# Kernel optimization log

Measured on AMD Instinct MI355X. Metric: run time of the kernel, lower is better.

Reference implementation:

```python
import jax, jax.numpy as jnp
import numpy as np

TAU = 0.07
EPS = 1e-6
N_SRC, N_TGT, D = 65536, 1024, 256
N_CLASSES = 345


def setup_inputs() -> dict:
    key = jax.random.key(0)
    k1, k2, k3 = jax.random.split(key, 3)
    source_features = jax.random.normal(k1, (N_SRC, D), dtype=jnp.float32)
    target_features = jax.random.normal(k2, (N_TGT, D), dtype=jnp.float32)
    source_labels = jax.random.randint(k3, (N_SRC,), 0, N_CLASSES)
    return {
        "source_features": source_features,
        "source_labels": source_labels,
        "target_features": target_features,
        "ranking_k": 5,
        "top_ranked_n": 512,
        "top_n_sim": 5,
    }


def _mode_along0(x):
    # torch.mode(dim=0): most frequent value; ties broken by smallest value.
    # x: [K, T] int. counts[i, t] = #{j : x[j,t] == x[i,t]}
    counts = (x[:, None, :] == x[None, :, :]).sum(axis=1)  # [K, T]
    # lexicographic key: maximize count, then minimize value
    score = counts.astype(jnp.int32) * 1000000 - x
    best = jnp.argmax(score, axis=0)  # [T]
    return jnp.take_along_axis(x, best[None, :], axis=0)[0]


def reference(source_features, source_labels, target_features, ranking_k, top_ranked_n, top_n_sim):
    # cosine similarity matrix [N_src, N_tgt]
    s = source_features / jnp.linalg.norm(source_features, axis=1, keepdims=True)
    t = target_features / jnp.linalg.norm(target_features, axis=1, keepdims=True)
    sim = s @ t.T

    # sort each column descending (over source axis)
    order = jnp.argsort(-sim, axis=0)                      # [Ns, Nt]
    sim_sorted = jnp.take_along_axis(sim, order, axis=0)   # [Ns, Nt]

    # kNN pseudo-label per target: mode of top_n_sim nearest source labels
    neigh = source_labels[order[:top_n_sim]]               # [K, Nt]
    assigned = _mode_along0(neigh)                         # [Nt]

    # per-target confidence score: sum of top-ranking_k same-label sims /
    #                              sum of top-ranking_k diff-label sims (in sorted order)
    lbl_sorted = source_labels[order]                      # [Ns, Nt]
    m = lbl_sorted == assigned[None, :]                    # [Ns, Nt] bool
    nln = jnp.where(m & (jnp.cumsum(m, axis=0) <= ranking_k), sim_sorted, 0.0).sum(axis=0)
    nm = ~m
    nun = jnp.where(nm & (jnp.cumsum(nm, axis=0) <= ranking_k), sim_sorted, 0.0).sum(axis=0)
    scores = jax.lax.stop_gradient(nln / nun)              # [Nt] (detached in original)

    # keep top_ranked_n most confident targets
    _, idx = jax.lax.top_k(scores, top_ranked_n)           # [Ntop]
    csim = sim[:, idx]                                     # [Ns, Ntop]
    clab = assigned[idx]                                   # [Ntop]

    # masked contrastive loss over source axis
    mask = (source_labels[:, None] == clab[None, :]).astype(csim.dtype)
    p = jax.nn.softmax(csim / TAU, axis=0)
    contrast = (p * mask).sum(axis=0) / p.sum(axis=0)
    return -jnp.mean(jnp.log(contrast + EPS))
```

## Files before the change

kernel.cpp:

```cpp
#include <hip/hip_runtime.h>
#include <cmath>
#include <cstdint>
#include <cstddef>
#include <climits>

#define N_SRC 65536
#define N_TGT 1024
#define DIM   256
#define TAU_INV (1.0f/0.07f)
#define LOSS_EPS 1e-6f
#define TOPSEL 512
#define N_CLASSES 345
#define SLICE_R 256
#define NS (N_SRC/SLICE_R)

typedef __bf16 bf16x8 __attribute__((ext_vector_type(8)));
typedef float  f32x4  __attribute__((ext_vector_type(4)));

__device__ __forceinline__ unsigned short f2bf(float x) {
  unsigned u = __float_as_uint(x);
  unsigned r = (u + 0x7fffu + ((u >> 16) & 1u)) >> 16;
  return (unsigned short)r;
}
__device__ __forceinline__ float bf2f(unsigned short h) {
  return __uint_as_float(((unsigned)h) << 16);
}

__device__ __forceinline__ void insert5_vi(float v[5], int id[5], float nv, int ni) {
  bool beats_last = (nv > v[4]) || (nv == v[4] && ni < id[4]);
  if (!beats_last) return;
  #pragma unroll
  for (int p = 4; p > 0; --p) {
    bool up = (nv > v[p-1]) || (nv == v[p-1] && ni < id[p-1]);
    if (up) { v[p] = v[p-1]; id[p] = id[p-1]; }
    else    { v[p] = nv; id[p] = ni; return; }
  }
  v[0] = nv; id[0] = ni;
}
__device__ __forceinline__ void insert5_v(float v[5], float nv) {
  if (!(nv > v[4])) return;
  #pragma unroll
  for (int p = 4; p > 0; --p) {
    if (nv > v[p-1]) v[p] = v[p-1];
    else { v[p] = nv; return; }
  }
  v[0] = nv;
}
__device__ __forceinline__ void wave_merge5_vi(float v[5], int id[5]) {
  #pragma unroll
  for (int off = 1; off < 64; off <<= 1) {
    float pv[5]; int pi[5];
    #pragma unroll
    for (int u = 0; u < 5; ++u) {
      pv[u] = __shfl_xor(v[u], off, 64);
      pi[u] = __shfl_xor(id[u], off, 64);
    }
    #pragma unroll
    for (int u = 0; u < 5; ++u) insert5_vi(v, id, pv[u], pi[u]);
  }
}
__device__ __forceinline__ void wave_merge5_v(float v[5]) {
  #pragma unroll
  for (int off = 1; off < 64; off <<= 1) {
    float pv[5];
    #pragma unroll
    for (int u = 0; u < 5; ++u) pv[u] = __shfl_xor(v[u], off, 64);
    #pragma unroll
    for (int u = 0; u < 5; ++u) insert5_v(v, pv[u]);
  }
}

__global__ __launch_bounds__(512) void k_zero(int* __restrict__ hist) {
  if (threadIdx.x < N_CLASSES) hist[threadIdx.x] = 0;
}
__global__ __launch_bounds__(256) void k_hist(const int* __restrict__ labels,
                                              int* __restrict__ hist) {
  int i = blockIdx.x * 256 + threadIdx.x;
  atomicAdd(&hist[labels[i]], 1);
}
__global__ __launch_bounds__(64) void k_scan(const int* __restrict__ hist,
                                             int* __restrict__ start,
                                             int* __restrict__ cursor) {
  if (threadIdx.x == 0) {
    int acc = 0;
    for (int c = 0; c < N_CLASSES; ++c) {
      start[c] = acc; cursor[c] = acc; acc += hist[c];
    }
    start[N_CLASSES] = acc;
  }
}
__global__ __launch_bounds__(256) void k_perm(const int* __restrict__ labels,
                                              int* __restrict__ cursor,
                                              int* __restrict__ g,
                                              int* __restrict__ sortedLab) {
  int i = blockIdx.x * 256 + threadIdx.x;
  int l = labels[i];
  int slot = atomicAdd(&cursor[l], 1);
  g[slot] = i;
  sortedLab[slot] = l;
}

__global__ __launch_bounds__(256) void k_norm_split(const float* __restrict__ X,
                                                    const int* __restrict__ g,
                                                    unsigned short* __restrict__ hi,
                                                    unsigned short* __restrict__ lo) {
  int wave = threadIdx.x >> 6, lane = threadIdx.x & 63;
  int row  = blockIdx.x * 4 + wave;
  int src  = g ? g[row] : row;
  float4 v = reinterpret_cast<const float4*>(X + (size_t)src * DIM)[lane];
  float ss = v.x*v.x + v.y*v.y + v.z*v.z + v.w*v.w;
  #pragma unroll
  for (int o = 32; o > 0; o >>= 1) ss += __shfl_xor(ss, o, 64);
  float r = 1.0f / sqrtf(ss);
  v.x *= r; v.y *= r; v.z *= r; v.w *= r;
  ushort4 h, l;
  h.x = f2bf(v.x); l.x = f2bf(v.x - bf2f(h.x));
  h.y = f2bf(v.y); l.y = f2bf(v.y - bf2f(h.y));
  h.z = f2bf(v.z); l.z = f2bf(v.z - bf2f(h.z));
  h.w = f2bf(v.w); l.w = f2bf(v.w - bf2f(h.w));
  reinterpret_cast<ushort4*>(hi + (size_t)row * DIM)[lane] = h;
  reinterpret_cast<ushort4*>(lo + (size_t)row * DIM)[lane] = l;
}

__device__ __forceinline__ void gl_lds(const unsigned short* g, unsigned short* d) {
  __builtin_amdgcn_global_load_lds(
      (const __attribute__((address_space(1))) unsigned int*)g,
      (__attribute__((address_space(3))) unsigned int*)d, 16, 0, 0);
}

__global__ __launch_bounds__(256) void k_gemm(
    const unsigned short* __restrict__ Ahi, const unsigned short* __restrict__ Alo,
    const unsigned short* __restrict__ Bhi, const unsigned short* __restrict__ Blo,
    float* __restrict__ simIJ, int cols, int j_off)
{
  __shared__ unsigned short As_hi[128*32];
  __shared__ unsigned short As_lo[128*32];
  __shared__ unsigned short Bs_hi[128*32];
  __shared__ unsigned short Bs_lo[128*32];

  const int tid  = threadIdx.x;
  const int lane = tid & 63;
  const int w    = tid >> 6;
  const int wm   = w & 1;
  const int wn   = w >> 1;
  const int i0   = blockIdx.x * 128;
  const int j0g  = j_off + blockIdx.y * 128;
  const int j0l  = blockIdx.y * 128;

  f32x4 acc[4][4];
  #pragma unroll
  for (int a = 0; a < 4; ++a)
    #pragma unroll
    for (int b = 0; b < 4; ++b) acc[a][b] = f32x4{0.f, 0.f, 0.f, 0.f};

  const int srow = (w << 5) + (lane >> 2);
  const int scol = (lane & 3) << 3;
  const unsigned short* gAh = Ahi + (size_t)(j0g + srow) * DIM + scol;
  const unsigned short* gAl = Alo + (size_t)(j0g + srow) * DIM + scol;
  const unsigned short* gBh = Bhi + (size_t)(i0  + srow) * DIM + scol;
  const unsigned short* gBl = Blo + (size_t)(i0  + srow) * DIM + scol;
  unsigned short* dA0  = &As_hi[(w << 5) * 32];
  unsigned short* dA1  = &As_hi[((w << 5) + 16) * 32];
  unsigned short* dB0  = &Bs_hi[(w << 5) * 32];
  unsigned short* dB1  = &Bs_hi[((w << 5) + 16) * 32];
  unsigned short* dA0l = &As_lo[(w << 5) * 32];
  unsigned short* dA1l = &As_lo[((w << 5) + 16) * 32];
  unsigned short* dB0l = &Bs_lo[(w << 5) * 32];
  unsigned short* dB1l = &Bs_lo[((w << 5) + 16) * 32];

  const int fr = lane & 15;
  const int fk = (lane >> 4) << 3;

  for (int k0 = 0; k0 < DIM; k0 += 32) {
    __syncthreads();
    gl_lds(gAh + k0,           dA0);
    gl_lds(gAh + k0 + 16*DIM,  dA1);
    gl_lds(gAl + k0,           dA0l);
    gl_lds(gAl + k0 + 16*DIM,  dA1l);
    gl_lds(gBh + k0,           dB0);
    gl_lds(gBh + k0 + 16*DIM,  dB1);
    gl_lds(gBl + k0,           dB0l);
    gl_lds(gBl + k0 + 16*DIM,  dB1l);
    __syncthreads();

    bf16x8 ah[4], al[4], bh[4], bl[4];
    #pragma unroll
    for (int rf = 0; rf < 4; ++rf) {
      int r = ((wm << 6) + (rf << 4) + fr) * 32 + fk;
      ah[rf] = *(const bf16x8*)&As_hi[r];
      al[rf] = *(const bf16x8*)&As_lo[r];
    }
    #pragma unroll
    for (int cf = 0; cf < 4; ++cf) {
      int r = ((wn << 6) + (cf << 4) + fr) * 32 + fk;
      bh[cf] = *(const bf16x8*)&Bs_hi[r];
      bl[cf] = *(const bf16x8*)&Bs_lo[r];
    }
    #pragma unroll
    for (int rf = 0; rf < 4; ++rf)
      #pragma unroll
      for (int cf = 0; cf < 4; ++cf) {
        acc[rf][cf] = __builtin_amdgcn_mfma_f32_16x16x32_bf16(ah[rf], bh[cf], acc[rf][cf], 0, 0, 0);
        acc[rf][cf] = __builtin_amdgcn_mfma_f32_16x16x32_bf16(ah[rf], bl[cf], acc[rf][cf], 0, 0, 0);
        acc[rf][cf] = __builtin_amdgcn_mfma_f32_16x16x32_bf16(al[rf], bh[cf], acc[rf][cf], 0, 0, 0);
      }
  }

  #pragma unroll
  for (int rf = 0; rf < 4; ++rf) {
    const int m_base = (wm << 6) + (rf << 4) + ((lane >> 4) << 2);
    #pragma unroll
    for (int cf = 0; cf < 4; ++cf) {
      const int n = (wn << 6) + (cf << 4) + (lane & 15);
      *reinterpret_cast<float4*>(&simIJ[(size_t)(i0 + n) * cols + j0l + m_base]) =
          make_float4(acc[rf][cf][0], acc[rf][cf][1], acc[rf][cf][2], acc[rf][cf][3]);
    }
  }
}

template<int CPT>
__global__ __launch_bounds__(512) void k_part1t(const float* __restrict__ sim,
                                                int cols,
                                                float* __restrict__ p1v,
                                                int* __restrict__ p1i,
                                                float* __restrict__ pse) {
  const int s  = blockIdx.x;
  const int t  = threadIdx.x;
  const int jc = t * CPT;
  if (jc >= cols) return;
  float tv0[5]; int ti0[5]; float se0 = 0.f;
  float tv1[5]; int ti1[5]; float se1 = 0.f;
  #pragma unroll
  for (int u = 0; u < 5; ++u) { tv0[u] = -INFINITY; ti0[u] = INT_MAX;
                                tv1[u] = -INFINITY; ti1[u] = INT_MAX; }
  const int i0 = s * SLICE_R;
  #pragma unroll 4
  for (int it = 0; it < SLICE_R; ++it) {
    const int i = i0 + it;
    if constexpr (CPT == 2) {
      float2 v = *reinterpret_cast<const float2*>(&sim[(size_t)i * cols + jc]);
      se0 += __expf(v.x * TAU_INV);
      se1 += __expf(v.y * TAU_INV);
      if (v.x > tv0[4]) insert5_vi(tv0, ti0, v.x, i);
      if (v.y > tv1[4]) insert5_vi(tv1, ti1, v.y, i);
    } else {
      float v = sim[(size_t)i * cols + jc];
      se0 += __expf(v * TAU_INV);
      if (v > tv0[4]) insert5_vi(tv0, ti0, v, i);
    }
  }
  {
    const size_t o = ((size_t)s * cols + jc) * 5;
    #pragma unroll
    for (int u = 0; u < 5; ++u) { p1v[o+u] = tv0[u]; p1i[o+u] = ti0[u]; }
    pse[(size_t)s * cols + jc] = se0;
  }
  if constexpr (CPT == 2) {
    const size_t o = ((size_t)s * cols + jc + 1) * 5;
    #pragma unroll
    for (int u = 0; u < 5; ++u) { p1v[o+u] = tv1[u]; p1i[o+u] = ti1[u]; }
    pse[(size_t)s * cols + jc + 1] = se1;
  }
}

__global__ __launch_bounds__(256) void k_assign(const float* __restrict__ p1v,
                                                const int* __restrict__ p1i,
                                                const int* __restrict__ sortedLab,
                                                int* __restrict__ assigned,
                                                int cols, int j_off) {
  const int w = threadIdx.x >> 6, lane = threadIdx.x & 63;
  const int jloc = blockIdx.x * 4 + w;
  float v[5]; int id[5];
  #pragma unroll
  for (int u = 0; u < 5; ++u) { v[u] = -INFINITY; id[u] = INT_MAX; }
  #pragma unroll
  for (int r = 0; r < NS/64; ++r) {
    const int s = r * 64 + lane;
    const size_t o = ((size_t)s * cols + jloc) * 5;
    #pragma unroll
    for (int u = 0; u < 5; ++u) insert5_vi(v, id, p1v[o+u], p1i[o+u]);
  }
  wave_merge5_vi(v, id);
  if (lane == 0) {
    int lab[5];
    #pragma unroll
    for (int a = 0; a < 5; ++a) lab[a] = sortedLab[id[a]];
    int bestSc = INT_MIN, bestA = 0;
    #pragma unroll
    for (int a = 0; a < 5; ++a) {
      int c = 0;
      #pragma unroll
      for (int b = 0; b < 5; ++b) c += (lab[b] == lab[a]) ? 1 : 0;
      int sc = c * 1000000 - lab[a];
      if (sc > bestSc) { bestSc = sc; bestA = a; }
    }
    assigned[j_off + jloc] = lab[bestA];
  }
}

__global__ __launch_bounds__(256) void k_part2n(const float* __restrict__ sim,
                                                const int* __restrict__ assigned,
                                                const int* __restrict__ start,
                                                const float* __restrict__ p1v,
                                                const float* __restrict__ pse,
                                                float* __restrict__ scores,
                                                float* __restrict__ contrast,
                                                int cols, int j_off) {
  const int w = threadIdx.x >> 6, lane = threadIdx.x & 63;
  const int jloc = blockIdx.x * 4 + w;
  const int j    = j_off + jloc;
  const int asg  = assigned[j];
  const int a    = start[asg];
  const int b    = start[asg + 1];
  const int s0   = a >> 8;
  const int s1   = (b - 1) >> 8;

  float mt[5], ut[5]; float sem = 0.f, se = 0.f;
  #pragma unroll
  for (int u = 0; u < 5; ++u) { mt[u] = -INFINITY; ut[u] = -INFINITY; }

  for (int i = s0 * SLICE_R + lane; i < (s1 + 1) * SLICE_R; i += 64) {
    float v = sim[(size_t)i * cols + jloc];
    if (i >= a && i < b) { sem += __expf(v * TAU_INV); insert5_v(mt, v); }
    else insert5_v(ut, v);
  }
  #pragma unroll
  for (int r = 0; r < NS/64; ++r) {
    const int s = r * 64 + lane;
    se += pse[(size_t)s * cols + jloc];
    if (s < s0 || s > s1) {
      const size_t o = ((size_t)s * cols + jloc) * 5;
      #pragma unroll
      for (int u = 0; u < 5; ++u) insert5_v(ut, p1v[o+u]);
    }
  }
  #pragma unroll
  for (int o = 32; o > 0; o >>= 1) { sem += __shfl_xor(sem, o, 64); se += __shfl_xor(se, o, 64); }
  wave_merge5_v(mt);
  wave_merge5_v(ut);
  if (lane == 0) {
    float nln = 0.f, nun = 0.f;
    #pragma unroll
    for (int u = 0; u < 5; ++u) {
      if (mt[u] > -1e30f) nln += mt[u];
      if (ut[u] > -1e30f) nun += ut[u];
    }
    scores[j]   = nln / nun;
    contrast[j] = sem / se;
  }
}

__global__ __launch_bounds__(1024) void k_finalize(const float* __restrict__ scores,
                                                   const float* __restrict__ contrast,
                                                   float* __restrict__ out) {
  __shared__ float sc[N_TGT];
  __shared__ float red[N_TGT];
  const int j = threadIdx.x;
  sc[j] = scores[j];
  __syncthreads();
  float my = sc[j];
  int rank = 0;
  for (int m = 0; m < N_TGT; ++m) {
    float s = sc[m];
    rank += ((s > my) || (s == my && m < j)) ? 1 : 0;
  }
  red[j] = (rank < TOPSEL) ? logf(contrast[j] + LOSS_EPS) : 0.0f;
  __syncthreads();
  for (int s = 512; s > 0; s >>= 1) { if (j < s) red[j] += red[j+s]; __syncthreads(); }
  if (j == 0) out[0] = -red[0] / (float)TOPSEL;
}

extern "C" void kernel_launch(void* const* d_in, const int* in_sizes, int n_in,
                              void* d_out, int out_size, void* d_ws, size_t ws_size,
                              hipStream_t stream) {
  const float* S      = (const float*)d_in[0];
  const int*   labels = (const int*)d_in[1];
  const float* T      = (const float*)d_in[2];
  float* out = (float*)d_out;

  float* ws = (float*)d_ws;
  float* scores    = ws;
  float* contrastA = scores + N_TGT;
  int*   assigned  = (int*)(contrastA + N_TGT);
  float* p1v       = (float*)(assigned + N_TGT);
  int*   p1i       = (int*)(p1v + (size_t)NS*N_TGT*5);
  float* pse       = (float*)(p1i + (size_t)NS*N_TGT*5);
  int*   hist      = (int*)(pse + (size_t)NS*N_TGT);
  int*   startArr  = hist + N_CLASSES;
  int*   cursor    = startArr + (N_CLASSES + 1);
  int*   gidx      = cursor + N_CLASSES;
  int*   sortedLab = gidx + N_SRC;
  unsigned short* Shi = (unsigned short*)(sortedLab + N_SRC);
  unsigned short* Slo = Shi + (size_t)N_SRC*DIM;
  unsigned short* Thi = Slo + (size_t)N_SRC*DIM;
  unsigned short* Tlo = Thi + (size_t)N_TGT*DIM;
  float* simbuf       = (float*)(Tlo + (size_t)N_TGT*DIM);

  size_t head  = (size_t)(simbuf - ws);
  size_t avail = (ws_size / 4 > head) ? (ws_size / 4 - head) : 0;
  int cols = 128;
  if      (avail >= (size_t)1024 * N_SRC) cols = 1024;
  else if (avail >= (size_t)512  * N_SRC) cols = 512;
  else if (avail >= (size_t)256  * N_SRC) cols = 256;

  k_zero<<<1, 512, 0, stream>>>(hist);
  k_hist<<<N_SRC/256, 256, 0, stream>>>(labels, hist);
  k_scan<<<1, 64, 0, stream>>>(hist, startArr, cursor);
  k_perm<<<N_SRC/256, 256, 0, stream>>>(labels, cursor, gidx, sortedLab);

  k_norm_split<<<N_TGT/4, 256, 0, stream>>>(T, nullptr, Thi, Tlo);
  k_norm_split<<<N_SRC/4, 256, 0, stream>>>(S, gidx, Shi, Slo);

  for (int j_off = 0; j_off < N_TGT; j_off += cols) {
    dim3 gg(N_SRC / 128, cols / 128);
    k_gemm<<<gg, 256, 0, stream>>>(Thi, Tlo, Shi, Slo, simbuf, cols, j_off);
    if (cols >= 1024)
      k_part1t<2><<<NS, 512, 0, stream>>>(simbuf, cols, p1v, p1i, pse);
    else
      k_part1t<1><<<NS, 512, 0, stream>>>(simbuf, cols, p1v, p1i, pse);
    k_assign<<<cols/4, 256, 0, stream>>>(p1v, p1i, sortedLab, assigned, cols, j_off);
    k_part2n<<<cols/4, 256, 0, stream>>>(simbuf, assigned, startArr, p1v, pse,
                                         scores, contrastA, cols, j_off);
  }
  k_finalize<<<1, 1024, 0, stream>>>(scores, contrastA, out);
}
```

Measured before the change: 1.098 ms.

## Shrink partial-reduction slices, swizzle GEMM block order, use one column per thread

```diff
diff --git a/kernel.cpp b/kernel.cpp
--- a/kernel.cpp
+++ b/kernel.cpp
@@ -11,7 +11,7 @@
 #define LOSS_EPS 1e-6f
 #define TOPSEL 512
 #define N_CLASSES 345
-#define SLICE_R 256
+#define SLICE_R 64
 #define NS (N_SRC/SLICE_R)
 
 typedef __bf16 bf16x8 __attribute__((ext_vector_type(8)));
@@ -143,9 +143,16 @@
   const int w    = tid >> 6;
   const int wm   = w & 1;
   const int wn   = w >> 1;
-  const int i0   = blockIdx.x * 128;
-  const int j0g  = j_off + blockIdx.y * 128;
-  const int j0l  = blockIdx.y * 128;
+
+  const int nby = cols >> 7;
+  const int d   = blockIdx.x;
+  const int c   = d & 7;
+  const int kk  = d >> 3;
+  const int by  = kk % nby;
+  const int bx  = (kk / nby) * 8 + c;
+  const int i0   = bx * 128;
+  const int j0g  = j_off + by * 128;
+  const int j0l  = by * 128;
 
   f32x4 acc[4][4];
   #pragma unroll
@@ -218,49 +225,28 @@
   }
 }
 
-template<int CPT>
-__global__ __launch_bounds__(512) void k_part1t(const float* __restrict__ sim,
-                                                int cols,
-                                                float* __restrict__ p1v,
-                                                int* __restrict__ p1i,
-                                                float* __restrict__ pse) {
+__global__ __launch_bounds__(1024) void k_part1t(const float* __restrict__ sim,
+                                                 int cols,
+                                                 float* __restrict__ p1v,
+                                                 int* __restrict__ p1i,
+                                                 float* __restrict__ pse) {
   const int s  = blockIdx.x;
-  const int t  = threadIdx.x;
-  const int jc = t * CPT;
-  if (jc >= cols) return;
+  const int jc = threadIdx.x;
   float tv0[5]; int ti0[5]; float se0 = 0.f;
-  float tv1[5]; int ti1[5]; float se1 = 0.f;
-  #pragma unroll
-  for (int u = 0; u < 5; ++u) { tv0[u] = -INFINITY; ti0[u] = INT_MAX;
-                                tv1[u] = -INFINITY; ti1[u] = INT_MAX; }
+  #pragma unroll
+  for (int u = 0; u < 5; ++u) { tv0[u] = -INFINITY; ti0[u] = INT_MAX; }
   const int i0 = s * SLICE_R;
-  #pragma unroll 4
+  const float* p = sim + (size_t)i0 * cols + jc;
+  #pragma unroll 8
   for (int it = 0; it < SLICE_R; ++it) {
-    const int i = i0 + it;
-    if constexpr (CPT == 2) {
-      float2 v = *reinterpret_cast<const float2*>(&sim[(size_t)i * cols + jc]);
-      se0 += __expf(v.x * TAU_INV);
-      se1 += __expf(v.y * TAU_INV);
-      if (v.x > tv0[4]) insert5_vi(tv0, ti0, v.x, i);
-      if (v.y > tv1[4]) insert5_vi(tv1, ti1, v.y, i);
-    } else {
-      float v = sim[(size_t)i * cols + jc];
-      se0 += __expf(v * TAU_INV);
-      if (v > tv0[4]) insert5_vi(tv0, ti0, v, i);
-    }
-  }
-  {
-    const size_t o = ((size_t)s * cols + jc) * 5;
-    #pragma unroll
-    for (int u = 0; u < 5; ++u) { p1v[o+u] = tv0[u]; p1i[o+u] = ti0[u]; }
-    pse[(size_t)s * cols + jc] = se0;
-  }
-  if constexpr (CPT == 2) {
-    const size_t o = ((size_t)s * cols + jc + 1) * 5;
-    #pragma unroll
-    for (int u = 0; u < 5; ++u) { p1v[o+u] = tv1[u]; p1i[o+u] = ti1[u]; }
-    pse[(size_t)s * cols + jc + 1] = se1;
-  }
+    float v = p[(size_t)it * cols];
+    se0 += __expf(v * TAU_INV);
+    if (v > tv0[4]) insert5_vi(tv0, ti0, v, i0 + it);
+  }
+  const size_t o = ((size_t)s * cols + jc) * 5;
+  #pragma unroll
+  for (int u = 0; u < 5; ++u) { p1v[o+u] = tv0[u]; p1i[o+u] = ti0[u]; }
+  pse[(size_t)s * cols + jc] = se0;
 }
 
 __global__ __launch_bounds__(256) void k_assign(const float* __restrict__ p1v,
@@ -312,8 +298,8 @@
   const int asg  = assigned[j];
   const int a    = start[asg];
   const int b    = start[asg + 1];
-  const int s0   = a >> 8;
-  const int s1   = (b - 1) >> 8;
+  const int s0   = a >> 6;
+  const int s1   = (b - 1) >> 6;
 
   float mt[5], ut[5]; float sem = 0.f, se = 0.f;
   #pragma unroll
@@ -412,12 +398,9 @@
   k_norm_split<<<N_SRC/4, 256, 0, stream>>>(S, gidx, Shi, Slo);
 
   for (int j_off = 0; j_off < N_TGT; j_off += cols) {
-    dim3 gg(N_SRC / 128, cols / 128);
-    k_gemm<<<gg, 256, 0, stream>>>(Thi, Tlo, Shi, Slo, simbuf, cols, j_off);
-    if (cols >= 1024)
-      k_part1t<2><<<NS, 512, 0, stream>>>(simbuf, cols, p1v, p1i, pse);
-    else
-      k_part1t<1><<<NS, 512, 0, stream>>>(simbuf, cols, p1v, p1i, pse);
+    k_gemm<<<(N_SRC/128) * (cols/128), 256, 0, stream>>>(Thi, Tlo, Shi, Slo,
+                                                         simbuf, cols, j_off);
+    k_part1t<<<NS, cols, 0, stream>>>(simbuf, cols, p1v, p1i, pse);
     k_assign<<<cols/4, 256, 0, stream>>>(p1v, p1i, sortedLab, assigned, cols, j_off);
     k_part2n<<<cols/4, 256, 0, stream>>>(simbuf, assigned, startArr, p1v, pse,
                                          scores, contrastA, cols, j_off);
```

Measured after the change: 1.034 ms. 1.06x faster.
